# Performance work log

Measured on AMD Instinct MI355X. Metric: run time of the kernel, lower is better.

## Reference

```python
import jax, jax.numpy as jnp
import numpy as np

SCALE = 1.0  # args.scale


def setup_inputs() -> dict:
    key = jax.random.key(0)
    k1, k2, k3, k4, k5 = jax.random.split(key, 5)
    B, S, D, R, LR = 4, 2048, 2048, 2048, 16  # batch, seq, column(emb), row(out), lora rank
    inp = jax.random.normal(k1, (B, S, D), dtype=jnp.float32)
    weight = jax.random.normal(k2, (R, D), dtype=jnp.float32) * (1.0 / np.sqrt(D))
    bias = jax.random.normal(k3, (R,), dtype=jnp.float32)
    lora_right = jax.random.normal(k4, (B, D, LR), dtype=jnp.float32) * 0.02
    lora_left = jax.random.normal(k5, (B, LR, R), dtype=jnp.float32) * 0.02
    return {"input": inp, "weight": weight, "bias": bias,
            "lora_right": lora_right, "lora_left": lora_left}


def reference(input, weight, bias, lora_right, lora_left):
    # Base linear: x @ W^T + b  -> [B, S, R]
    x = jnp.einsum('bsd,rd->bsr', input, weight) + bias
    # Per-sample low-rank LoRA chain: (input @ right) @ left, batched
    t = jnp.einsum('bsd,bdk->bsk', input, lora_right)   # [B, S, LR]
    y = jnp.einsum('bsk,bkr->bsr', t, lora_left)        # [B, S, R]
    # L2-normalize each token vector along the last dim, then scale
    y = y / jnp.linalg.norm(y, axis=-1, keepdims=True)
    y = y * SCALE
    return x + y
```

## Files before the change

kernel.cpp:

```cpp
#include <hip/hip_runtime.h>
#include <hip/hip_bf16.h>

#define SCALE_V 1.0f

typedef __bf16 bf16v8 __attribute__((ext_vector_type(8)));
typedef float f32v4 __attribute__((ext_vector_type(4)));

typedef const __attribute__((address_space(1))) void* gas_t;
typedef __attribute__((address_space(3))) void* las_t;
#define ASYNC_COPY16(g, l) \
    __builtin_amdgcn_global_load_lds((gas_t)(g), (las_t)(l), 16, 0, 0)
#define FENCE() asm volatile("" ::: "memory")
#define MFMA __builtin_amdgcn_mfma_f32_16x16x32_bf16

__global__ __launch_bounds__(256) void transpose_lr_kernel(
    const float* __restrict__ lright, float* __restrict__ lrT) {
    __shared__ float tile[16][273];
    const int b = blockIdx.y;
    const int d0 = blockIdx.x * 256;
    const int t = threadIdx.x;
    const float* src = lright + (size_t)b * 32768 + (size_t)d0 * 16;
    #pragma unroll
    for (int j = 0; j < 16; ++j) {
        tile[t & 15][j * 16 + (t >> 4)] = src[j * 256 + t];
    }
    __syncthreads();
    const int k = t >> 4, dcol = t & 15;
    float* dst = lrT + (size_t)b * 32768 + (size_t)k * 2048 + d0;
    #pragma unroll
    for (int j = 0; j < 16; ++j) {
        dst[dcol + j * 16] = tile[k][dcol + j * 16];
    }
}

__global__ __launch_bounds__(256) void prep_kernel(
    const float* __restrict__ inp, const float* __restrict__ wgt,
    const float* __restrict__ lrT, const float* __restrict__ lleft,
    __bf16* __restrict__ abf, __bf16* __restrict__ wbf,
    float* __restrict__ tout, float* __restrict__ gpart) {
    __shared__ float sm[256];
    const int bid = blockIdx.x;
    const int tid = threadIdx.x;

    if (bid < 2048) {
        const int row0 = bid * 4;
        const int b = row0 >> 11;
        const float* lt = lrT + (size_t)b * 32768;

        float x[4][8];
        #pragma unroll
        for (int rr = 0; rr < 4; ++rr) {
            const float* p = inp + (size_t)(row0 + rr) * 2048 + tid * 8;
            float4 a0 = *(const float4*)p;
            float4 a1 = *(const float4*)(p + 4);
            x[rr][0] = a0.x; x[rr][1] = a0.y; x[rr][2] = a0.z; x[rr][3] = a0.w;
            x[rr][4] = a1.x; x[rr][5] = a1.y; x[rr][6] = a1.z; x[rr][7] = a1.w;
            bf16v8 v;
            #pragma unroll
            for (int i = 0; i < 8; ++i) v[i] = (__bf16)x[rr][i];
            *(bf16v8*)(abf + (size_t)(row0 + rr) * 2048 + tid * 8) = v;
        }

        float v[64];
        #pragma unroll
        for (int k = 0; k < 16; ++k) {
            const float* lp = lt + (size_t)k * 2048 + tid * 8;
            float4 l0 = *(const float4*)lp;
            float4 l1 = *(const float4*)(lp + 4);
            float lv[8] = {l0.x, l0.y, l0.z, l0.w, l1.x, l1.y, l1.z, l1.w};
            #pragma unroll
            for (int rr = 0; rr < 4; ++rr) {
                float s = 0.f;
                #pragma unroll
                for (int i = 0; i < 8; ++i) s += x[rr][i] * lv[i];
                v[rr * 16 + k] = s;
            }
        }

        const int lane = tid & 63;
        const int w = tid >> 6;
        #pragma unroll
        for (int s = 1, cnt = 64; s < 64; s <<= 1, cnt >>= 1) {
            const int half = cnt >> 1;
            const bool up = (lane & s) != 0;
            #pragma unroll
            for (int i = 0; i < 32; ++i) {
                if (i < half) {
                    float keep = up ? v[i + half] : v[i];
                    float give = up ? v[i] : v[i + half];
                    v[i] = keep + __shfl_xor(give, s, 64);
                }
            }
        }
        const int rev = ((lane & 1) << 5) | ((lane & 2) << 3) | ((lane & 4) << 1) |
                        ((lane & 8) >> 1) | ((lane & 16) >> 3) | ((lane & 32) >> 5);
        sm[w * 64 + rev] = v[0];
        __syncthreads();
        if (tid < 64) {
            tout[(size_t)row0 * 16 + tid] =
                sm[tid] + sm[64 + tid] + sm[128 + tid] + sm[192 + tid];
        }
    } else if (bid < 4096) {
        const int i = ((bid - 2048) * 256 + tid) * 8;
        float4 x0 = *(const float4*)(wgt + i);
        float4 x1 = *(const float4*)(wgt + i + 4);
        bf16v8 v;
        v[0] = (__bf16)x0.x; v[1] = (__bf16)x0.y; v[2] = (__bf16)x0.z; v[3] = (__bf16)x0.w;
        v[4] = (__bf16)x1.x; v[5] = (__bf16)x1.y; v[6] = (__bf16)x1.z; v[7] = (__bf16)x1.w;
        *(bf16v8*)(wbf + i) = v;
    } else {
        const int g = bid - 4096;
        const int b = g >> 3, c = g & 7;
        const int k = tid >> 4, j = tid & 15;
        const float* pk = lleft + ((size_t)b * 16 + k) * 2048 + c * 256;
        const float* pj = lleft + ((size_t)b * 16 + j) * 2048 + c * 256;
        float s = 0.f;
        #pragma unroll 4
        for (int r = 0; r < 256; r += 4) {
            float4 a = *(const float4*)(pk + r);
            float4 d = *(const float4*)(pj + r);
            s += a.x * d.x + a.y * d.y + a.z * d.z + a.w * d.w;
        }
        gpart[((size_t)b * 8 + c) * 256 + tid] = s;
    }
}

__global__ __launch_bounds__(256) void norm_kernel(
    const float* __restrict__ gpart, float* __restrict__ t) {
    __shared__ float gs[256];
    const int tid = threadIdx.x;
    const int tok0 = blockIdx.x * 256;
    const int b = tok0 >> 11;
    float g = 0.f;
    #pragma unroll
    for (int c = 0; c < 8; ++c) g += gpart[((size_t)b * 8 + c) * 256 + tid];
    gs[tid] = g;
    __syncthreads();

    float* tp = t + (size_t)(tok0 + tid) * 16;
    float tv[16];
    {
        float4 a0 = *(const float4*)(tp);
        float4 a1 = *(const float4*)(tp + 4);
        float4 a2 = *(const float4*)(tp + 8);
        float4 a3 = *(const float4*)(tp + 12);
        tv[0]=a0.x; tv[1]=a0.y; tv[2]=a0.z; tv[3]=a0.w;
        tv[4]=a1.x; tv[5]=a1.y; tv[6]=a1.z; tv[7]=a1.w;
        tv[8]=a2.x; tv[9]=a2.y; tv[10]=a2.z; tv[11]=a2.w;
        tv[12]=a3.x; tv[13]=a3.y; tv[14]=a3.z; tv[15]=a3.w;
    }
    float q = 0.f;
    #pragma unroll
    for (int k = 0; k < 16; ++k) {
        float s = 0.f;
        #pragma unroll
        for (int j = 0; j < 16; ++j) s += gs[k * 16 + j] * tv[j];
        q += tv[k] * s;
    }
    const float r = SCALE_V * rsqrtf(q);
    float4 o;
    o.x = tv[0]*r;  o.y = tv[1]*r;  o.z = tv[2]*r;  o.w = tv[3]*r;  *(float4*)(tp)      = o;
    o.x = tv[4]*r;  o.y = tv[5]*r;  o.z = tv[6]*r;  o.w = tv[7]*r;  *(float4*)(tp + 4)  = o;
    o.x = tv[8]*r;  o.y = tv[9]*r;  o.z = tv[10]*r; o.w = tv[11]*r; *(float4*)(tp + 8)  = o;
    o.x = tv[12]*r; o.y = tv[13]*r; o.z = tv[14]*r; o.w = tv[15]*r; *(float4*)(tp + 12) = o;
}

__global__ __launch_bounds__(512, 2) void gemm_ep_kernel(
    const __bf16* __restrict__ abf, const __bf16* __restrict__ wbf,
    const float* __restrict__ bias, const float* __restrict__ tpr,
    const float* __restrict__ lleft, float* __restrict__ out) {
    __shared__ __attribute__((aligned(16))) char smem[131072];

    const int tid  = threadIdx.x;
    const int w    = tid >> 6;
    const int lane = tid & 63;
    const int l3   = lane >> 3, l7 = lane & 7;
    const int wm   = w >> 2;
    const int wn   = w & 3;
    const int fr   = lane & 15;

    const int xcd   = blockIdx.x & 7;
    const int local = blockIdx.x >> 3;
    const int tile_n = local & 7;
    const int tile_m = (xcd << 2) | (local >> 3);
    const int row0 = tile_m * 256;
    const int col0 = tile_n * 256;

    const int cswz = ((l7 ^ l3) * 8);
    const size_t aG0 = (size_t)(row0 + 8 * w + l3) * 2048 + cswz;
    const int bCh = 64 * (w >> 2) + 8 * (w & 3);
    const size_t bG0 = (size_t)(col0 + bCh + l3) * 2048 + cswz;
    char* const aDst = smem + 8 * w * 128 + lane * 16;
    char* const bDst = smem + 65536 + bCh * 128 + lane * 16;

#define STAGE_A(BUFOFF, S, KKEL)                                                         \
    do {                                                                                 \
        ASYNC_COPY16(abf + aG0 + (size_t)((S)*64) * 2048 + (KKEL),  aDst + (BUFOFF) + (S)*8192);          \
        ASYNC_COPY16(abf + aG0 + (size_t)((S)*64 + 128) * 2048 + (KKEL), aDst + (BUFOFF) + (S)*8192 + 16384); \
    } while (0)
#define STAGE_B(BUFOFF, S, KKEL)                                                         \
    do {                                                                                 \
        ASYNC_COPY16(wbf + bG0 + (size_t)((S)*32) * 2048 + (KKEL),  bDst + (BUFOFF) + (S)*4096);          \
        ASYNC_COPY16(wbf + bG0 + (size_t)((S)*32 + 128) * 2048 + (KKEL), bDst + (BUFOFF) + (S)*4096 + 16384); \
    } while (0)

    const int kx0 = (((lane >> 4) * 16) ^ (l7 << 4));
    const int kx1 = ((64 + (lane >> 4) * 16) ^ (l7 << 4));
    const char* const aRd = smem + (wm * 128 + fr) * 128;
    const char* const bRd = smem + 65536 + (wn * 64 + fr) * 128;

    f32v4 acc[8][4];
    #pragma unroll
    for (int m = 0; m < 8; ++m)
        #pragma unroll
        for (int n = 0; n < 4; ++n) {
            acc[m][n][0] = 0.f; acc[m][n][1] = 0.f;
            acc[m][n][2] = 0.f; acc[m][n][3] = 0.f;
        }

    STAGE_A(0, 0, 0);
    STAGE_B(0, 0, 0);
    STAGE_B(0, 1, 0);
    STAGE_A(0, 1, 0);
    STAGE_B(32768, 0, 64);
    STAGE_B(32768, 1, 64);
    STAGE_A(32768, 0, 64);
    asm volatile("s_waitcnt vmcnt(8)" ::: "memory");
    FENCE(); __builtin_amdgcn_s_barrier(); FENCE();

    for (int kt = 0; kt < 32; ++kt) {
        const int bo = (kt & 1) * 32768;
        const int bn = bo ^ 32768;
        const size_t kk1 = (size_t)((kt + 1) & 31) * 64;
        const size_t kk2 = (size_t)((kt + 2) & 31) * 64;
        bf16v8 af[4][2], bl[2][2], bh[2][2];

        #pragma unroll
        for (int m = 0; m < 4; ++m) {
            af[m][0] = *(const bf16v8*)(aRd + bo + m * 2048 + kx0);
            af[m][1] = *(const bf16v8*)(aRd + bo + m * 2048 + kx1);
        }
        #pragma unroll
        for (int n = 0; n < 2; ++n) {
            bl[n][0] = *(const bf16v8*)(bRd + bo + n * 2048 + kx0);
            bl[n][1] = *(const bf16v8*)(bRd + bo + n * 2048 + kx1);
        }
        STAGE_A(bn, 1, kk1);
        FENCE(); __builtin_amdgcn_s_barrier(); FENCE();
        __builtin_amdgcn_s_setprio(1);
        #pragma unroll
        for (int m = 0; m < 4; ++m)
            #pragma unroll
            for (int n = 0; n < 2; ++n) {
                acc[m][n] = MFMA(af[m][0], bl[n][0], acc[m][n], 0, 0, 0);
                acc[m][n] = MFMA(af[m][1], bl[n][1], acc[m][n], 0, 0, 0);
            }
        __builtin_amdgcn_s_setprio(0);
        FENCE(); __builtin_amdgcn_s_barrier(); FENCE();

        #pragma unroll
        for (int n = 0; n < 2; ++n) {
            bh[n][0] = *(const bf16v8*)(bRd + bo + (n + 2) * 2048 + kx0);
            bh[n][1] = *(const bf16v8*)(bRd + bo + (n + 2) * 2048 + kx1);
        }
        STAGE_B(bo, 0, kk2);
        asm volatile("s_waitcnt vmcnt(10)" ::: "memory");
        FENCE(); __builtin_amdgcn_s_barrier(); FENCE();
        __builtin_amdgcn_s_setprio(1);
        #pragma unroll
        for (int m = 0; m < 4; ++m)
            #pragma unroll
            for (int n = 0; n < 2; ++n) {
                acc[m][n + 2] = MFMA(af[m][0], bh[n][0], acc[m][n + 2], 0, 0, 0);
                acc[m][n + 2] = MFMA(af[m][1], bh[n][1], acc[m][n + 2], 0, 0, 0);
            }
        __builtin_amdgcn_s_setprio(0);
        FENCE(); __builtin_amdgcn_s_barrier(); FENCE();

        #pragma unroll
        for (int m = 0; m < 4; ++m) {
            af[m][0] = *(const bf16v8*)(aRd + bo + (m + 4) * 2048 + kx0);
            af[m][1] = *(const bf16v8*)(aRd + bo + (m + 4) * 2048 + kx1);
        }
        STAGE_B(bo, 1, kk2);
        FENCE(); __builtin_amdgcn_s_barrier(); FENCE();
        __builtin_amdgcn_s_setprio(1);
        #pragma unroll
        for (int m = 0; m < 4; ++m)
            #pragma unroll
            for (int n = 0; n < 2; ++n) {
                acc[m + 4][n + 2] = MFMA(af[m][0], bh[n][0], acc[m + 4][n + 2], 0, 0, 0);
                acc[m + 4][n + 2] = MFMA(af[m][1], bh[n][1], acc[m + 4][n + 2], 0, 0, 0);
            }
        __builtin_amdgcn_s_setprio(0);
        FENCE(); __builtin_amdgcn_s_barrier(); FENCE();

        STAGE_A(bo, 0, kk2);
        asm volatile("s_waitcnt vmcnt(8)" ::: "memory");
        FENCE(); __builtin_amdgcn_s_barrier(); FENCE();
        __builtin_amdgcn_s_setprio(1);
        #pragma unroll
        for (int m = 0; m < 4; ++m)
            #pragma unroll
            for (int n = 0; n < 2; ++n) {
                acc[m + 4][n] = MFMA(af[m][0], bl[n][0], acc[m + 4][n], 0, 0, 0);
                acc[m + 4][n] = MFMA(af[m][1], bl[n][1], acc[m + 4][n], 0, 0, 0);
            }
        __builtin_amdgcn_s_setprio(0);
        FENCE(); __builtin_amdgcn_s_barrier(); FENCE();
    }

    asm volatile("s_waitcnt vmcnt(0)" ::: "memory");
    __syncthreads();
    {
        const int r = tid >> 1;
        const int h = (tid & 1) * 8;
        bf16v8 zv;
        #pragma unroll
        for (int i = 0; i < 8; ++i) zv[i] = (__bf16)0.f;

        __bf16* tE = (__bf16*)smem;
        __bf16* LE = (__bf16*)(smem + 20480);

        const float* tp = tpr + (size_t)(row0 + r) * 16 + h;
        float4 t0 = *(const float4*)tp;
        float4 t1 = *(const float4*)(tp + 4);
        bf16v8 tv;
        tv[0]=(__bf16)t0.x; tv[1]=(__bf16)t0.y; tv[2]=(__bf16)t0.z; tv[3]=(__bf16)t0.w;
        tv[4]=(__bf16)t1.x; tv[5]=(__bf16)t1.y; tv[6]=(__bf16)t1.z; tv[7]=(__bf16)t1.w;
        *(bf16v8*)(tE + r * 40 + h) = tv;
        *(bf16v8*)(tE + r * 40 + 16 + h) = zv;

        const int bb = row0 >> 11;
        const float* lp = lleft + ((size_t)bb * 16 + h) * 2048 + col0 + r;
        bf16v8 lv;
        #pragma unroll
        for (int i = 0; i < 8; ++i) lv[i] = (__bf16)lp[(size_t)i * 2048];
        *(bf16v8*)(LE + r * 40 + h) = lv;
        *(bf16v8*)(LE + r * 40 + 16 + h) = zv;
    }
    __syncthreads();
    {
        const __bf16* tE = (const __bf16*)smem;
        const __bf16* LE = (const __bf16*)(smem + 20480);
        const int ko = (lane >> 4) * 8;
        bf16v8 bE[4];
        #pragma unroll
        for (int n = 0; n < 4; ++n)
            bE[n] = *(const bf16v8*)(LE + (wn * 64 + n * 16 + fr) * 40 + ko);
        #pragma unroll
        for (int m = 0; m < 8; ++m) {
            bf16v8 aE = *(const bf16v8*)(tE + (wm * 128 + m * 16 + fr) * 40 + ko);
            #pragma unroll
            for (int n = 0; n < 4; ++n)
                acc[m][n] = MFMA(aE, bE[n], acc[m][n], 0, 0, 0);
        }
    }

    #pragma unroll
    for (int n = 0; n < 4; ++n) {
        const int gc = col0 + wn * 64 + n * 16 + fr;
        const float bv = bias[gc];
        #pragma unroll
        for (int m = 0; m < 8; ++m) {
            #pragma unroll
            for (int j = 0; j < 4; ++j) {
                const int gr = row0 + wm * 128 + m * 16 + (lane >> 4) * 4 + j;
                out[(size_t)gr * 2048 + gc] = acc[m][n][j] + bv;
            }
        }
    }
#undef STAGE_A
#undef STAGE_B
}

extern "C" void kernel_launch(void* const* d_in, const int* in_sizes, int n_in,
                              void* d_out, int out_size, void* d_ws, size_t ws_size,
                              hipStream_t stream) {
    const float* inp  = (const float*)d_in[0];
    const float* wgt  = (const float*)d_in[1];
    const float* bias = (const float*)d_in[2];
    const float* lrt  = (const float*)d_in[3];
    const float* llf  = (const float*)d_in[4];
    float* out = (float*)d_out;

    char* ws = (char*)d_ws;
    __bf16* abf  = (__bf16*)ws;
    __bf16* wbf  = (__bf16*)(ws + 33554432);
    float*  tbuf = (float*)(ws + 41943040);
    float*  gprt = (float*)(ws + 42467328);
    float*  lrT  = (float*)(ws + 42500096);

    transpose_lr_kernel<<<dim3(8, 4), 256, 0, stream>>>(lrt, lrT);
    prep_kernel<<<4128, 256, 0, stream>>>(inp, wgt, lrT, llf, abf, wbf, tbuf, gprt);
    norm_kernel<<<32, 256, 0, stream>>>(gprt, tbuf);
    gemm_ep_kernel<<<dim3(256), 512, 0, stream>>>(abf, wbf, bias, tbuf, llf, out);
}
```

Before: 111.8 us.

## Shrink GEMM tile to 128x256 with K=32 double buffer for higher occupancy

Rewrites the main bf16 GEMM to use 128x256 output tiles with a K-step of 32 and a simpler double-buffered async-copy loop. Shared memory per block drops to 48KB and the launch bound asks for 4 blocks per CU, with twice as many blocks launched. The goal is to hide latency through occupancy instead of the hand-scheduled multi-phase pipeline. In exchange, each tile reuses less data (more global and LDS traffic per FLOP), takes twice as many K iterations with a barrier in each, and the new swizzle for 64-byte rows may cause bank conflicts.

Measured after the change: 122.1 us. 1.09x slower.

```diff
diff --git a/kernel.cpp b/kernel.cpp
--- a/kernel.cpp
+++ b/kernel.cpp
@@ -165,16 +165,15 @@
     o.x = tv[12]*r; o.y = tv[13]*r; o.z = tv[14]*r; o.w = tv[15]*r; *(float4*)(tp + 12) = o;
 }
 
-__global__ __launch_bounds__(512, 2) void gemm_ep_kernel(
+__global__ __launch_bounds__(512, 4) void gemm_ep_kernel(
     const __bf16* __restrict__ abf, const __bf16* __restrict__ wbf,
     const float* __restrict__ bias, const float* __restrict__ tpr,
     const float* __restrict__ lleft, float* __restrict__ out) {
-    __shared__ __attribute__((aligned(16))) char smem[131072];
+    __shared__ __attribute__((aligned(16))) char smem[49152];
 
     const int tid  = threadIdx.x;
     const int w    = tid >> 6;
     const int lane = tid & 63;
-    const int l3   = lane >> 3, l7 = lane & 7;
     const int wm   = w >> 2;
     const int wn   = w & 3;
     const int fr   = lane & 15;
@@ -182,175 +181,117 @@
     const int xcd   = blockIdx.x & 7;
     const int local = blockIdx.x >> 3;
     const int tile_n = local & 7;
-    const int tile_m = (xcd << 2) | (local >> 3);
-    const int row0 = tile_m * 256;
+    const int tile_m = (xcd << 3) | (local >> 3);
+    const int row0 = tile_m * 128;
     const int col0 = tile_n * 256;
 
-    const int cswz = ((l7 ^ l3) * 8);
-    const size_t aG0 = (size_t)(row0 + 8 * w + l3) * 2048 + cswz;
-    const int bCh = 64 * (w >> 2) + 8 * (w & 3);
-    const size_t bG0 = (size_t)(col0 + bCh + l3) * 2048 + cswz;
-    char* const aDst = smem + 8 * w * 128 + lane * 16;
-    char* const bDst = smem + 65536 + bCh * 128 + lane * 16;
-
-#define STAGE_A(BUFOFF, S, KKEL)                                                         \
-    do {                                                                                 \
-        ASYNC_COPY16(abf + aG0 + (size_t)((S)*64) * 2048 + (KKEL),  aDst + (BUFOFF) + (S)*8192);          \
-        ASYNC_COPY16(abf + aG0 + (size_t)((S)*64 + 128) * 2048 + (KKEL), aDst + (BUFOFF) + (S)*8192 + 16384); \
+    const int swzel = ((tid & 3) ^ ((tid >> 3) & 3)) * 8;
+    const __bf16* const aSrc  = abf + (size_t)(row0 + (tid >> 2)) * 2048 + swzel;
+    const __bf16* const bSrc0 = wbf + (size_t)(col0 + (tid >> 2)) * 2048 + swzel;
+    const __bf16* const bSrc1 = bSrc0 + (size_t)128 * 2048;
+    char* const aD  = smem + tid * 16;
+    char* const bD0 = smem + 16384 + tid * 16;
+    char* const bD1 = smem + 16384 + 8192 + tid * 16;
+
+#define STAGE3(AOFF, BOFF, KKEL)                        \
+    do {                                                \
+        ASYNC_COPY16(aSrc  + (KKEL), aD  + (AOFF));     \
+        ASYNC_COPY16(bSrc0 + (KKEL), bD0 + (BOFF));     \
+        ASYNC_COPY16(bSrc1 + (KKEL), bD1 + (BOFF));     \
     } while (0)
-#define STAGE_B(BUFOFF, S, KKEL)                                                         \
-    do {                                                                                 \
-        ASYNC_COPY16(wbf + bG0 + (size_t)((S)*32) * 2048 + (KKEL),  bDst + (BUFOFF) + (S)*4096);          \
-        ASYNC_COPY16(wbf + bG0 + (size_t)((S)*32 + 128) * 2048 + (KKEL), bDst + (BUFOFF) + (S)*4096 + 16384); \
-    } while (0)
-
-    const int kx0 = (((lane >> 4) * 16) ^ (l7 << 4));
-    const int kx1 = ((64 + (lane >> 4) * 16) ^ (l7 << 4));
-    const char* const aRd = smem + (wm * 128 + fr) * 128;
-    const char* const bRd = smem + 65536 + (wn * 64 + fr) * 128;
-
-    f32v4 acc[8][4];
-    #pragma unroll
-    for (int m = 0; m < 8; ++m)
+
+    const int kx = (((lane >> 4) ^ ((fr >> 1) & 3)) * 16);
+    const char* const aRdB = smem + (wm * 64 + fr) * 64 + kx;
+    const char* const bRdB = smem + 16384 + (wn * 64 + fr) * 64 + kx;
+
+    f32v4 acc[4][4];
+    #pragma unroll
+    for (int m = 0; m < 4; ++m)
         #pragma unroll
         for (int n = 0; n < 4; ++n) {
             acc[m][n][0] = 0.f; acc[m][n][1] = 0.f;
             acc[m][n][2] = 0.f; acc[m][n][3] = 0.f;
         }
 
-    STAGE_A(0, 0, 0);
-    STAGE_B(0, 0, 0);
-    STAGE_B(0, 1, 0);
-    STAGE_A(0, 1, 0);
-    STAGE_B(32768, 0, 64);
-    STAGE_B(32768, 1, 64);
-    STAGE_A(32768, 0, 64);
-    asm volatile("s_waitcnt vmcnt(8)" ::: "memory");
+    STAGE3(0, 0, 0);
+    STAGE3(8192, 16384, 32);
+    asm volatile("s_waitcnt vmcnt(3)" ::: "memory");
     FENCE(); __builtin_amdgcn_s_barrier(); FENCE();
 
-    for (int kt = 0; kt < 32; ++kt) {
-        const int bo = (kt & 1) * 32768;
-        const int bn = bo ^ 32768;
-        const size_t kk1 = (size_t)((kt + 1) & 31) * 64;
-        const size_t kk2 = (size_t)((kt + 2) & 31) * 64;
-        bf16v8 af[4][2], bl[2][2], bh[2][2];
-
-        #pragma unroll
-        for (int m = 0; m < 4; ++m) {
-            af[m][0] = *(const bf16v8*)(aRd + bo + m * 2048 + kx0);
-            af[m][1] = *(const bf16v8*)(aRd + bo + m * 2048 + kx1);
-        }
-        #pragma unroll
-        for (int n = 0; n < 2; ++n) {
-            bl[n][0] = *(const bf16v8*)(bRd + bo + n * 2048 + kx0);
-            bl[n][1] = *(const bf16v8*)(bRd + bo + n * 2048 + kx1);
-        }
-        STAGE_A(bn, 1, kk1);
+    #pragma unroll 2
+    for (int kt = 0; kt < 64; ++kt) {
+        const int aOff = (kt & 1) * 8192;
+        const int bOff = (kt & 1) * 16384;
+        const int kk2 = ((kt + 2) & 63) * 32;
+
+        bf16v8 af[4], bfr[4];
+        #pragma unroll
+        for (int m = 0; m < 4; ++m)
+            af[m] = *(const bf16v8*)(aRdB + aOff + m * 1024);
+        #pragma unroll
+        for (int n = 0; n < 4; ++n)
+            bfr[n] = *(const bf16v8*)(bRdB + bOff + n * 1024);
+
+        __builtin_amdgcn_s_setprio(1);
+        #pragma unroll
+        for (int m = 0; m < 4; ++m)
+            #pragma unroll
+            for (int n = 0; n < 4; ++n)
+                acc[m][n] = MFMA(af[m], bfr[n], acc[m][n], 0, 0, 0);
+        __builtin_amdgcn_s_setprio(0);
+
         FENCE(); __builtin_amdgcn_s_barrier(); FENCE();
-        __builtin_amdgcn_s_setprio(1);
-        #pragma unroll
-        for (int m = 0; m < 4; ++m)
-            #pragma unroll
-            for (int n = 0; n < 2; ++n) {
-                acc[m][n] = MFMA(af[m][0], bl[n][0], acc[m][n], 0, 0, 0);
-                acc[m][n] = MFMA(af[m][1], bl[n][1], acc[m][n], 0, 0, 0);
-            }
-        __builtin_amdgcn_s_setprio(0);
-        FENCE(); __builtin_amdgcn_s_barrier(); FENCE();
-
-        #pragma unroll
-        for (int n = 0; n < 2; ++n) {
-            bh[n][0] = *(const bf16v8*)(bRd + bo + (n + 2) * 2048 + kx0);
-            bh[n][1] = *(const bf16v8*)(bRd + bo + (n + 2) * 2048 + kx1);
-        }
-        STAGE_B(bo, 0, kk2);
-        asm volatile("s_waitcnt vmcnt(10)" ::: "memory");
-        FENCE(); __builtin_amdgcn_s_barrier(); FENCE();
-        __builtin_amdgcn_s_setprio(1);
-        #pragma unroll
-        for (int m = 0; m < 4; ++m)
-            #pragma unroll
-            for (int n = 0; n < 2; ++n) {
-                acc[m][n + 2] = MFMA(af[m][0], bh[n][0], acc[m][n + 2], 0, 0, 0);
-                acc[m][n + 2] = MFMA(af[m][1], bh[n][1], acc[m][n + 2], 0, 0, 0);
-            }
-        __builtin_amdgcn_s_setprio(0);
-        FENCE(); __builtin_amdgcn_s_barrier(); FENCE();
-
-        #pragma unroll
-        for (int m = 0; m < 4; ++m) {
-            af[m][0] = *(const bf16v8*)(aRd + bo + (m + 4) * 2048 + kx0);
-            af[m][1] = *(const bf16v8*)(aRd + bo + (m + 4) * 2048 + kx1);
-        }
-        STAGE_B(bo, 1, kk2);
-        FENCE(); __builtin_amdgcn_s_barrier(); FENCE();
-        __builtin_amdgcn_s_setprio(1);
-        #pragma unroll
-        for (int m = 0; m < 4; ++m)
-            #pragma unroll
-            for (int n = 0; n < 2; ++n) {
-                acc[m + 4][n + 2] = MFMA(af[m][0], bh[n][0], acc[m + 4][n + 2], 0, 0, 0);
-                acc[m + 4][n + 2] = MFMA(af[m][1], bh[n][1], acc[m + 4][n + 2], 0, 0, 0);
-            }
-        __builtin_amdgcn_s_setprio(0);
-        FENCE(); __builtin_amdgcn_s_barrier(); FENCE();
-
-        STAGE_A(bo, 0, kk2);
-        asm volatile("s_waitcnt vmcnt(8)" ::: "memory");
-        FENCE(); __builtin_amdgcn_s_barrier(); FENCE();
-        __builtin_amdgcn_s_setprio(1);
-        #pragma unroll
-        for (int m = 0; m < 4; ++m)
-            #pragma unroll
-            for (int n = 0; n < 2; ++n) {
-                acc[m + 4][n] = MFMA(af[m][0], bl[n][0], acc[m + 4][n], 0, 0, 0);
-                acc[m + 4][n] = MFMA(af[m][1], bl[n][1], acc[m + 4][n], 0, 0, 0);
-            }
-        __builtin_amdgcn_s_setprio(0);
+        STAGE3(aOff, bOff, kk2);
+        asm volatile("s_waitcnt vmcnt(3)" ::: "memory");
         FENCE(); __builtin_amdgcn_s_barrier(); FENCE();
     }
 
     asm volatile("s_waitcnt vmcnt(0)" ::: "memory");
     __syncthreads();
     {
-        const int r = tid >> 1;
-        const int h = (tid & 1) * 8;
         bf16v8 zv;
         #pragma unroll
         for (int i = 0; i < 8; ++i) zv[i] = (__bf16)0.f;
 
         __bf16* tE = (__bf16*)smem;
-        __bf16* LE = (__bf16*)(smem + 20480);
-
-        const float* tp = tpr + (size_t)(row0 + r) * 16 + h;
-        float4 t0 = *(const float4*)tp;
-        float4 t1 = *(const float4*)(tp + 4);
-        bf16v8 tv;
-        tv[0]=(__bf16)t0.x; tv[1]=(__bf16)t0.y; tv[2]=(__bf16)t0.z; tv[3]=(__bf16)t0.w;
-        tv[4]=(__bf16)t1.x; tv[5]=(__bf16)t1.y; tv[6]=(__bf16)t1.z; tv[7]=(__bf16)t1.w;
-        *(bf16v8*)(tE + r * 40 + h) = tv;
-        *(bf16v8*)(tE + r * 40 + 16 + h) = zv;
-
-        const int bb = row0 >> 11;
-        const float* lp = lleft + ((size_t)bb * 16 + h) * 2048 + col0 + r;
-        bf16v8 lv;
-        #pragma unroll
-        for (int i = 0; i < 8; ++i) lv[i] = (__bf16)lp[(size_t)i * 2048];
-        *(bf16v8*)(LE + r * 40 + h) = lv;
-        *(bf16v8*)(LE + r * 40 + 16 + h) = zv;
+        __bf16* LE = (__bf16*)(smem + 10240);
+
+        if (tid < 256) {
+            const int r = tid >> 1;
+            const int h = (tid & 1) * 8;
+            const float* tp = tpr + (size_t)(row0 + r) * 16 + h;
+            float4 t0 = *(const float4*)tp;
+            float4 t1 = *(const float4*)(tp + 4);
+            bf16v8 tv;
+            tv[0]=(__bf16)t0.x; tv[1]=(__bf16)t0.y; tv[2]=(__bf16)t0.z; tv[3]=(__bf16)t0.w;
+            tv[4]=(__bf16)t1.x; tv[5]=(__bf16)t1.y; tv[6]=(__bf16)t1.z; tv[7]=(__bf16)t1.w;
+            *(bf16v8*)(tE + r * 40 + h) = tv;
+            *(bf16v8*)(tE + r * 40 + 16 + h) = zv;
+        }
+        {
+            const int r = tid >> 1;
+            const int h = (tid & 1) * 8;
+            const int bb = row0 >> 11;
+            const float* lp = lleft + ((size_t)bb * 16 + h) * 2048 + col0 + r;
+            bf16v8 lv;
+            #pragma unroll
+            for (int i = 0; i < 8; ++i) lv[i] = (__bf16)lp[(size_t)i * 2048];
+            *(bf16v8*)(LE + r * 40 + h) = lv;
+            *(bf16v8*)(LE + r * 40 + 16 + h) = zv;
+        }
     }
     __syncthreads();
     {
         const __bf16* tE = (const __bf16*)smem;
-        const __bf16* LE = (const __bf16*)(smem + 20480);
+        const __bf16* LE = (const __bf16*)(smem + 10240);
         const int ko = (lane >> 4) * 8;
         bf16v8 bE[4];
         #pragma unroll
         for (int n = 0; n < 4; ++n)
             bE[n] = *(const bf16v8*)(LE + (wn * 64 + n * 16 + fr) * 40 + ko);
         #pragma unroll
-        for (int m = 0; m < 8; ++m) {
-            bf16v8 aE = *(const bf16v8*)(tE + (wm * 128 + m * 16 + fr) * 40 + ko);
+        for (int m = 0; m < 4; ++m) {
+            bf16v8 aE = *(const bf16v8*)(tE + (wm * 64 + m * 16 + fr) * 40 + ko);
             #pragma unroll
             for (int n = 0; n < 4; ++n)
                 acc[m][n] = MFMA(aE, bE[n], acc[m][n], 0, 0, 0);
@@ -362,16 +303,15 @@
         const int gc = col0 + wn * 64 + n * 16 + fr;
         const float bv = bias[gc];
         #pragma unroll
-        for (int m = 0; m < 8; ++m) {
+        for (int m = 0; m < 4; ++m) {
             #pragma unroll
             for (int j = 0; j < 4; ++j) {
-                const int gr = row0 + wm * 128 + m * 16 + (lane >> 4) * 4 + j;
+                const int gr = row0 + wm * 64 + m * 16 + (lane >> 4) * 4 + j;
                 out[(size_t)gr * 2048 + gc] = acc[m][n][j] + bv;
             }
         }
     }
-#undef STAGE_A
-#undef STAGE_B
+#undef STAGE3
 }
 
 extern "C" void kernel_launch(void* const* d_in, const int* in_sizes, int n_in,
@@ -394,5 +334,5 @@
     transpose_lr_kernel<<<dim3(8, 4), 256, 0, stream>>>(lrt, lrT);
     prep_kernel<<<4128, 256, 0, stream>>>(inp, wgt, lrT, llf, abf, wbf, tbuf, gprt);
     norm_kernel<<<32, 256, 0, stream>>>(gprt, tbuf);
-    gemm_ep_kernel<<<dim3(256), 512, 0, stream>>>(abf, wbf, bias, tbuf, llf, out);
-}
+    gemm_ep_kernel<<<dim3(512), 512, 0, stream>>>(abf, wbf, bias, tbuf, llf, out);
+}
```
